# Optimization experiments

Hardware: AMD Instinct MI355X
Metric: run time of the kernel (lower is better)

## Reference

```python
import jax, jax.numpy as jnp
import numpy as np
import math

H = 0.1
SHIFTS = (1, 2, 4, 8)
INTERACTION_SCALE = 0.05
DEXP_ORDER = 4
EXP_TERMS = 8
BERNOULLI = (1.0, -0.5, 1.0 / 6.0, 0.0, -1.0 / 30.0)


def _gp_table():
    # Cl(3,0) geometric product structure constants, basis [1,e1,e2,e3,e12,e13,e23,e123]
    def sign(a, b):
        a >>= 1
        total = 0
        while a:
            total += bin(a & b).count('1')
            a >>= 1
        return -1.0 if total & 1 else 1.0
    masks = [0b000, 0b001, 0b010, 0b100, 0b011, 0b101, 0b110, 0b111]
    idx = {m: i for i, m in enumerate(masks)}
    M = np.zeros((8, 8, 8), np.float32)
    for i, a in enumerate(masks):
        for j, b in enumerate(masks):
            M[i, j, idx[a ^ b]] = sign(a, b)
    return M

GP_TABLE = jnp.asarray(_gp_table())


def gp(a, b):
    # Clifford geometric product over the trailing 8-dim multivector axis
    return jnp.einsum('...i,ijk,...j->...k', a, GP_TABLE, b)


def clifford_exp(u, terms=EXP_TERMS):
    ident = jnp.zeros_like(u).at[..., 0].set(1.0)
    res, term = ident, ident
    for n in range(1, terms):
        term = gp(term, u) / float(n)
        res = res + term
    return res


def dexp_inv(u, w, order=DEXP_ORDER):
    # dexp^{-1}_u(w) = sum_k B_k/k! * ad_u^k(w)
    res = BERNOULLI[0] * w
    adw = w
    for k in range(1, order + 1):
        adw = gp(u, adw) - gp(adw, u)
        c = BERNOULLI[k] / math.factorial(k)
        if c != 0.0:
            res = res + c * adw
    return res


def derivative_fn(y, t):
    # harmonic-oscillator phase-space field: dq = p, dp = -q
    d = jnp.zeros_like(y)
    d = d.at[..., 1:4].set(y[..., 4:7])
    d = d.at[..., 4:7].set(-y[..., 1:4])
    return d


def rolling_interaction(y):
    accum = jnp.zeros_like(y)
    for s in SHIFTS:
        accum = accum + gp(y, jnp.roll(y, -s, axis=-2)) / float(s)
    return INTERACTION_SCALE * accum / float(len(SHIFTS))


def vector_field(y, t):
    return derivative_fn(y, t) + rolling_interaction(y)


def left_multiply(u, y):
    return gp(clifford_exp(u), y)


def step(y, t, dt):
    zero = jnp.zeros_like(y)
    k1 = dexp_inv(zero, vector_field(left_multiply(zero, y), t))
    u2 = 0.5 * dt * k1
    k2 = dexp_inv(u2, vector_field(left_multiply(u2, y), t + 0.5 * dt))
    u3 = 0.5 * dt * k2
    k3 = dexp_inv(u3, vector_field(left_multiply(u3, y), t + 0.5 * dt))
    u4 = dt * k3
    k4 = dexp_inv(u4, vector_field(left_multiply(u4, y), t + dt))
    u = dt * (k1 + 2.0 * k2 + 2.0 * k3 + k4) / 6.0
    u = jnp.clip(jnp.nan_to_num(u, nan=0.0, posinf=1.0, neginf=-1.0), -1.0, 1.0)
    return left_multiply(u, y)


def setup_inputs() -> dict:
    key = jax.random.key(0)
    y = jax.random.normal(key, (32, 65536, 8), dtype=jnp.float32)
    t = jnp.zeros((), dtype=jnp.float32)
    return {"y": y, "t": t}


def reference(y, t):
    return step(y, t, jnp.asarray(H, dtype=y.dtype))
```

## Files before the change

kernel.cpp:

```cpp
#include <hip/hip_runtime.h>
#include <math.h>

#define CC   256
#define SP   8
#define NY   (CC + 33)
#define NZ   (CC + 25)
#define NK2  (CC + 17)
#define NK3  (CC + 9)
#define ISCL 0.0125f


__device__ __forceinline__ void cmul(float& orr, float& oi,
                                     float ar, float ai, float br, float bi) {
    orr = fmaf(ar, br, -(ai * bi));
    oi  = fmaf(ar, bi,   ai * br);
}
__device__ __forceinline__ void cmad(float& orr, float& oi,
                                     float ar, float ai, float br, float bi) {
    orr = fmaf(ar, br, fmaf(-ai, bi, orr));
    oi  = fmaf(ar, bi, fmaf( ai, br, oi));
}
__device__ __forceinline__ void cmsub(float& orr, float& oi,
                                      float ar, float ai, float br, float bi) {
    orr = fmaf(-ar, br, fmaf( ai, bi, orr));
    oi  = fmaf(-ar, bi, fmaf(-ai, br, oi));
}

__device__ __forceinline__ void mm2(const float* a, const float* b, float* o) {
    float r0,r1,r2,r3,r4,r5,r6,r7;
    cmul(r0,r1, a[0],a[1], b[0],b[1]); cmad(r0,r1, a[2],a[3], b[4],b[5]);
    cmul(r2,r3, a[0],a[1], b[2],b[3]); cmad(r2,r3, a[2],a[3], b[6],b[7]);
    cmul(r4,r5, a[4],a[5], b[0],b[1]); cmad(r4,r5, a[6],a[7], b[4],b[5]);
    cmul(r6,r7, a[4],a[5], b[2],b[3]); cmad(r6,r7, a[6],a[7], b[6],b[7]);
    o[0]=r0; o[1]=r1; o[2]=r2; o[3]=r3; o[4]=r4; o[5]=r5; o[6]=r6; o[7]=r7;
}

__device__ __forceinline__ void comm_core2(const float* u6,
        float w01r, float w01i, float w10r, float w10i,
        float dwr, float dwi, float* o6) {
    const float dar = 2.f * u6[0], dai = 2.f * u6[1];
    float ar, ai;
    cmul (ar, ai, u6[2],u6[3], w10r,w10i);
    cmsub(ar, ai, u6[4],u6[5], w01r,w01i);
    o6[0] = ar; o6[1] = ai;
    cmul (ar, ai, w01r,w01i, dar,dai);
    cmsub(ar, ai, u6[2],u6[3], dwr,dwi);
    o6[2] = ar; o6[3] = ai;
    cmul (ar, ai, u6[4],u6[5], dwr,dwi);
    cmsub(ar, ai, w10r,w10i, dar,dai);
    o6[4] = ar; o6[5] = ai;
}

__device__ __forceinline__ void dexpinv8(const float* k, const float* w,
                                         float s, float* o) {
    float u6[6];
    u6[0] = 0.5f*(k[0]-k[6]); u6[1] = 0.5f*(k[1]-k[7]);
    u6[2] = k[2]; u6[3] = k[3]; u6[4] = k[4]; u6[5] = k[5];
    float a1[6], a2[6];
    comm_core2(u6, w[2],w[3], w[4],w[5], w[0]-w[6], w[1]-w[7], a1);
    comm_core2(u6, a1[2],a1[3], a1[4],a1[5], 2.f*a1[0], 2.f*a1[1], a2);
    float wkr = fmaf(u6[0],u6[0], -(u6[1]*u6[1]));
    wkr = fmaf(u6[2], u6[4], wkr); wkr = fmaf(-u6[3], u6[5], wkr);
    float wki = 2.f*u6[0]*u6[1];
    wki = fmaf(u6[2], u6[5], wki); wki = fmaf(u6[3], u6[4], wki);
    const float s2  = s*s;
    const float c1  = -0.5f*s;
    const float c2  = s2*(1.f/12.f);
    const float c4m = -(s2*s2)*(1.f/180.f);
    const float gr = fmaf(c4m, wkr, c2), gi = c4m*wki;
    float acc[6];
#pragma unroll
    for (int p = 0; p < 3; ++p) {
        const float a2r = a2[2*p], a2i = a2[2*p+1];
        acc[2*p]   = fmaf(gr, a2r, fmaf(-gi, a2i, c1*a1[2*p]));
        acc[2*p+1] = fmaf(gr, a2i, fmaf( gi, a2r, c1*a1[2*p+1]));
    }
    o[0] = w[0] + acc[0]; o[1] = w[1] + acc[1];
    o[2] = w[2] + acc[2]; o[3] = w[3] + acc[3];
    o[4] = w[4] + acc[4]; o[5] = w[5] + acc[5];
    o[6] = w[6] - acc[0]; o[7] = w[7] - acc[1];
}

__device__ __forceinline__ void chstep(float& pr, float& pi,
                                       float wr, float wi, float K) {
    const float nr = fmaf(pr, wr, fmaf(-pi, wi, K));
    const float ni = fmaf(pr, wi, pi * wr);
    pr = nr; pi = ni;
}
template<bool FULL>
__device__ __forceinline__ void expm(const float* k, float s, float* o) {
    const float hs = 0.5f * s;
    const float c0r = hs*(k[0]+k[6]), c0i = hs*(k[1]+k[7]);
    const float v0r = hs*(k[0]-k[6]), v0i = hs*(k[1]-k[7]);
    const float v1r = s*k[2], v1i = s*k[3];
    const float v2r = s*k[4], v2i = s*k[5];
    float wr = fmaf(v0r, v0r, -(v0i*v0i));
    wr = fmaf(v1r, v2r, wr); wr = fmaf(-v1i, v2i, wr);
    float wi = 2.f*v0r*v0i;
    wi = fmaf(v1r, v2i, wi); wi = fmaf(v1i, v2r, wi);
    float Cr, Ci = 0.f, Sr, Si = 0.f;
    if (FULL) {
        Cr = 1.f/40320.f;
        chstep(Cr, Ci, wr, wi, 1.f/720.f);
        chstep(Cr, Ci, wr, wi, 1.f/24.f);
        chstep(Cr, Ci, wr, wi, 0.5f);
        chstep(Cr, Ci, wr, wi, 1.f);
        Sr = 1.f/362880.f;
        chstep(Sr, Si, wr, wi, 1.f/5040.f);
        chstep(Sr, Si, wr, wi, 1.f/120.f);
        chstep(Sr, Si, wr, wi, 1.f/6.f);
        chstep(Sr, Si, wr, wi, 1.f);
    } else {
        Cr = 1.f/24.f;
        chstep(Cr, Ci, wr, wi, 0.5f);
        chstep(Cr, Ci, wr, wi, 1.f);
        Sr = 1.f/120.f;
        chstep(Sr, Si, wr, wi, 1.f/6.f);
        chstep(Sr, Si, wr, wi, 1.f);
    }
    const float ex = __expf(c0r);
    const float cs = __cosf(c0i), sn = __sinf(c0i);
    const float er = ex*cs, ei = ex*sn;
    float p0r, p0i; cmul(p0r, p0i, Sr, Si, v0r, v0i);
    const float tr = Cr + p0r, ti = Ci + p0i;
    const float ur = Cr - p0r, ui = Ci - p0i;
    cmul(o[0], o[1], er, ei, tr, ti);
    cmul(o[6], o[7], er, ei, ur, ui);
    float qr, qi; cmul(qr, qi, er, ei, Sr, Si);
    cmul(o[2], o[3], qr, qi, v1r, v1i);
    cmul(o[4], o[5], qr, qi, v2r, v2i);
}

__device__ __forceinline__ int sbase(int e) { return (e << 3) ^ (e & 4); }

__device__ __forceinline__ void lds_load8(const float* buf, int e, float* o) {
    const int b = sbase(e);
    float4 a = *(const float4*)(buf + b);
    float4 c = *(const float4*)(buf + (b ^ 4));
    o[0] = a.x; o[1] = a.y; o[2] = a.z; o[3] = a.w;
    o[4] = c.x; o[5] = c.y; o[6] = c.z; o[7] = c.w;
}
__device__ __forceinline__ void lds_store8(float* buf, int e, const float* v) {
    const int b = sbase(e);
    *(float4*)(buf + b)       = make_float4(v[0], v[1], v[2], v[3]);
    *(float4*)(buf + (b ^ 4)) = make_float4(v[4], v[5], v[6], v[7]);
}

__device__ __forceinline__ void vf8_lds(const float* buf, int e, float* o) {
    float z0[8], t1[8], t2[8], t4[8], t8[8], bc[8], g[8];
    lds_load8(buf, e,     z0);
    lds_load8(buf, e + 1, t1);
    lds_load8(buf, e + 2, t2);
    lds_load8(buf, e + 4, t4);
    lds_load8(buf, e + 8, t8);
#pragma unroll
    for (int c = 0; c < 8; ++c)
        bc[c] = fmaf(0.125f, t8[c], fmaf(0.25f, t4[c], fmaf(0.5f, t2[c], t1[c])));
    mm2(z0, bc, g);
    const float Sr  = z0[2]+z0[4], Si  = z0[3]+z0[5];
    const float Ddr = z0[0]-z0[6], Ddi = z0[1]-z0[7];
    const float Tr  = z0[4]-z0[2], Ti  = z0[5]-z0[3];
    o[0] = fmaf(ISCL, g[0],  0.5f*Si);
    o[1] = fmaf(ISCL, g[1], -0.5f*Sr);
    o[2] = fmaf(ISCL, g[2],  0.5f*(Ddi+Ti));
    o[3] = fmaf(ISCL, g[3], -0.5f*(Ddr+Tr));
    o[4] = fmaf(ISCL, g[4],  0.5f*(Ddi-Ti));
    o[5] = fmaf(ISCL, g[5], -0.5f*(Ddr-Tr));
    o[6] = fmaf(ISCL, g[6], -0.5f*Si);
    o[7] = fmaf(ISCL, g[7],  0.5f*Sr);
}

__device__ __forceinline__ void zstage(const float* ybuf, float* zbuf, int e,
                                       const float* k, float scale) {
    float ex[8], yv[8], o[8];
    expm<false>(k, scale, ex);
    lds_load8(ybuf, e, yv);
    mm2(ex, yv, o);
    lds_store8(zbuf, e, o);
}

__device__ __forceinline__ void kstage(const float* zbuf, int e,
                                       const float* kin, float scale, float* kout) {
    float w[8];
    vf8_lds(zbuf, e, w);
    dexpinv8(kin, w, scale, kout);
}

__global__ __launch_bounds__(CC, 4)
void clifford_step_kernel(const float* __restrict__ y, float* __restrict__ out) {
    __shared__ __align__(16) float sy[NY * SP];
    __shared__ __align__(16) float sz[NZ * SP];

    const int tid   = threadIdx.x;
    const int row   = blockIdx.x >> 8;
    const int chunk = blockIdx.x & 255;
    const int base  = chunk * CC;
    const int bt    = (tid - ((blockIdx.x & 3) << 6)) & 255;
    const float* __restrict__ yrow = y + (size_t)row * 65536u * 8u;

    {
        const int g0 = (base + tid) & 65535;
        const float4* p = (const float4*)(yrow + (size_t)g0 * 8u);
        float4 A = p[0], B = p[1];
        const int s = sbase(tid);
        *(float4*)&sy[s]     = make_float4(A.x + A.w, B.w + B.x, A.y - B.y, B.z - A.z);
        *(float4*)&sy[s ^ 4] = make_float4(A.y + B.y, B.z + A.z, A.x - A.w, B.w - B.x);
        if (bt < NY - CC) {
            const int e  = CC + bt;
            const int g1 = (base + e) & 65535;
            const float4* q = (const float4*)(yrow + (size_t)g1 * 8u);
            float4 Cv = q[0], D = q[1];
            const int s2 = sbase(e);
            *(float4*)&sy[s2]     = make_float4(Cv.x + Cv.w, D.w + D.x, Cv.y - D.y, D.z - Cv.z);
            *(float4*)&sy[s2 ^ 4] = make_float4(Cv.y + D.y, D.z + Cv.z, Cv.x - Cv.w, D.w - D.x);
        }
    }
    __syncthreads();

    float ka[8], kb[8], uacc[8], kn[8];

    vf8_lds(sy, tid, ka);
#pragma unroll
    for (int c = 0; c < 8; ++c) uacc[c] = ka[c];
    if (bt < NZ - CC) vf8_lds(sy, CC + bt, kb);

    zstage(sy, sz, tid, ka, 0.05f);
    if (bt < NZ - CC) zstage(sy, sz, CC + bt, kb, 0.05f);
    __syncthreads();

    kstage(sz, tid, ka, 0.05f, kn);
#pragma unroll
    for (int c = 0; c < 8; ++c) { ka[c] = kn[c]; uacc[c] = fmaf(2.f, kn[c], uacc[c]); }
    if (bt < NK2 - CC) {
        kstage(sz, CC + bt, kb, 0.05f, kn);
#pragma unroll
        for (int c = 0; c < 8; ++c) kb[c] = kn[c];
    }
    __syncthreads();

    zstage(sy, sz, tid, ka, 0.05f);
    if (bt < NK2 - CC) zstage(sy, sz, CC + bt, kb, 0.05f);
    __syncthreads();

    kstage(sz, tid, ka, 0.05f, kn);
#pragma unroll
    for (int c = 0; c < 8; ++c) { ka[c] = kn[c]; uacc[c] = fmaf(2.f, kn[c], uacc[c]); }
    if (bt < NK3 - CC) {
        kstage(sz, CC + bt, kb, 0.05f, kn);
#pragma unroll
        for (int c = 0; c < 8; ++c) kb[c] = kn[c];
    }
    __syncthreads();

    zstage(sy, sz, tid, ka, 0.1f);
    if (bt < NK3 - CC) zstage(sy, sz, CC + bt, kb, 0.1f);
    __syncthreads();

    {
        const int e = tid;
        float w[8], k4[8], um[8], ex[8], yv[8], om[8];
        vf8_lds(sz, e, w);
        dexpinv8(ka, w, 0.1f, k4);

        const float s6 = 0.1f / 6.0f;
#pragma unroll
        for (int c = 0; c < 8; ++c)
            um[c] = s6 * (uacc[c] + k4[c]);
        float av[8];
        av[0] = 0.5f*(um[0]+um[6]); av[3] = 0.5f*(um[0]-um[6]);
        av[7] = 0.5f*(um[1]+um[7]); av[4] = 0.5f*(um[1]-um[7]);
        av[1] = 0.5f*(um[2]+um[4]); av[5] = 0.5f*(um[4]-um[2]);
        av[6] = 0.5f*(um[3]+um[5]); av[2] = 0.5f*(um[5]-um[3]);
#pragma unroll
        for (int c = 0; c < 8; ++c) {
            float v = av[c];
            if (isnan(v)) v = 0.f;
            av[c] = fmaxf(-1.f, fminf(v, 1.f));
        }
        um[0] = av[0]+av[3]; um[1] = av[7]+av[4];
        um[2] = av[1]-av[5]; um[3] = av[6]-av[2];
        um[4] = av[1]+av[5]; um[5] = av[6]+av[2];
        um[6] = av[0]-av[3]; um[7] = av[7]-av[4];

        expm<true>(um, 1.f, ex);
        lds_load8(sy, e, yv);
        mm2(ex, yv, om);

        float* dst = out + ((size_t)row * 65536u + (size_t)(base + e)) * 8u;
        ((float4*)dst)[0] = make_float4(0.5f*(om[0]+om[6]), 0.5f*(om[2]+om[4]),
                                        0.5f*(om[5]-om[3]), 0.5f*(om[0]-om[6]));
        ((float4*)dst)[1] = make_float4(0.5f*(om[1]-om[7]), 0.5f*(om[4]-om[2]),
                                        0.5f*(om[3]+om[5]), 0.5f*(om[1]+om[7]));
    }
}

extern "C" void kernel_launch(void* const* d_in, const int* in_sizes, int n_in,
                              void* d_out, int out_size, void* d_ws, size_t ws_size,
                              hipStream_t stream) {
    const float* y = (const float*)d_in[0];
    float* out = (float*)d_out;
    dim3 grid(32 * 256);
    dim3 block(CC);
    hipLaunchKernelGGL(clifford_step_kernel, grid, block, 0, stream, y, out);
}
```

Measured before the change: 83.50 us.

## Double-buffer stage LDS to drop barriers, approximate scalar exp, stream shift loads

```diff
diff --git a/kernel.cpp b/kernel.cpp
--- a/kernel.cpp
+++ b/kernel.cpp
@@ -99,6 +99,7 @@
     float wi = 2.f*v0r*v0i;
     wi = fmaf(v1r, v2i, wi); wi = fmaf(v1i, v2r, wi);
     float Cr, Ci = 0.f, Sr, Si = 0.f;
+    float er, ei;
     if (FULL) {
         Cr = 1.f/40320.f;
         chstep(Cr, Ci, wr, wi, 1.f/720.f);
@@ -110,6 +111,9 @@
         chstep(Sr, Si, wr, wi, 1.f/120.f);
         chstep(Sr, Si, wr, wi, 1.f/6.f);
         chstep(Sr, Si, wr, wi, 1.f);
+        const float ex = __expf(c0r);
+        er = ex * __cosf(c0i);
+        ei = ex * __sinf(c0i);
     } else {
         Cr = 1.f/24.f;
         chstep(Cr, Ci, wr, wi, 0.5f);
@@ -117,10 +121,13 @@
         Sr = 1.f/120.f;
         chstep(Sr, Si, wr, wi, 1.f/6.f);
         chstep(Sr, Si, wr, wi, 1.f);
-    }
-    const float ex = __expf(c0r);
-    const float cs = __cosf(c0i), sn = __sinf(c0i);
-    const float er = ex*cs, ei = ex*sn;
+        float t1r = fmaf(c0r, 1.f/3.f, 1.f), t1i = c0i * (1.f/3.f);
+        float t2r, t2i;
+        cmul(t2r, t2i, t1r, t1i, c0r, c0i);
+        t2r = fmaf(0.5f, t2r, 1.f); t2i *= 0.5f;
+        cmul(er, ei, t2r, t2i, c0r, c0i);
+        er += 1.f;
+    }
     float p0r, p0i; cmul(p0r, p0i, Sr, Si, v0r, v0i);
     const float tr = Cr + p0r, ti = Ci + p0i;
     const float ur = Cr - p0r, ui = Ci - p0i;
@@ -147,15 +154,18 @@
 }
 
 __device__ __forceinline__ void vf8_lds(const float* buf, int e, float* o) {
-    float z0[8], t1[8], t2[8], t4[8], t8[8], bc[8], g[8];
+    float z0[8], bc[8], t[8], g[8];
     lds_load8(buf, e,     z0);
-    lds_load8(buf, e + 1, t1);
-    lds_load8(buf, e + 2, t2);
-    lds_load8(buf, e + 4, t4);
-    lds_load8(buf, e + 8, t8);
-#pragma unroll
-    for (int c = 0; c < 8; ++c)
-        bc[c] = fmaf(0.125f, t8[c], fmaf(0.25f, t4[c], fmaf(0.5f, t2[c], t1[c])));
+    lds_load8(buf, e + 1, bc);
+    lds_load8(buf, e + 2, t);
+#pragma unroll
+    for (int c = 0; c < 8; ++c) bc[c] = fmaf(0.5f, t[c], bc[c]);
+    lds_load8(buf, e + 4, t);
+#pragma unroll
+    for (int c = 0; c < 8; ++c) bc[c] = fmaf(0.25f, t[c], bc[c]);
+    lds_load8(buf, e + 8, t);
+#pragma unroll
+    for (int c = 0; c < 8; ++c) bc[c] = fmaf(0.125f, t[c], bc[c]);
     mm2(z0, bc, g);
     const float Sr  = z0[2]+z0[4], Si  = z0[3]+z0[5];
     const float Ddr = z0[0]-z0[6], Ddi = z0[1]-z0[7];
@@ -188,8 +198,9 @@
 
 __global__ __launch_bounds__(CC, 4)
 void clifford_step_kernel(const float* __restrict__ y, float* __restrict__ out) {
-    __shared__ __align__(16) float sy[NY * SP];
-    __shared__ __align__(16) float sz[NZ * SP];
+    __shared__ __align__(16) float sy [NY  * SP];
+    __shared__ __align__(16) float szA[NZ  * SP];
+    __shared__ __align__(16) float szB[NK2 * SP];
 
     const int tid   = threadIdx.x;
     const int row   = blockIdx.x >> 8;
@@ -223,43 +234,38 @@
 #pragma unroll
     for (int c = 0; c < 8; ++c) uacc[c] = ka[c];
     if (bt < NZ - CC) vf8_lds(sy, CC + bt, kb);
-
-    zstage(sy, sz, tid, ka, 0.05f);
-    if (bt < NZ - CC) zstage(sy, sz, CC + bt, kb, 0.05f);
+    zstage(sy, szA, tid, ka, 0.05f);
+    if (bt < NZ - CC) zstage(sy, szA, CC + bt, kb, 0.05f);
     __syncthreads();
 
-    kstage(sz, tid, ka, 0.05f, kn);
+    kstage(szA, tid, ka, 0.05f, kn);
 #pragma unroll
     for (int c = 0; c < 8; ++c) { ka[c] = kn[c]; uacc[c] = fmaf(2.f, kn[c], uacc[c]); }
     if (bt < NK2 - CC) {
-        kstage(sz, CC + bt, kb, 0.05f, kn);
+        kstage(szA, CC + bt, kb, 0.05f, kn);
 #pragma unroll
         for (int c = 0; c < 8; ++c) kb[c] = kn[c];
     }
+    zstage(sy, szB, tid, ka, 0.05f);
+    if (bt < NK2 - CC) zstage(sy, szB, CC + bt, kb, 0.05f);
     __syncthreads();
 
-    zstage(sy, sz, tid, ka, 0.05f);
-    if (bt < NK2 - CC) zstage(sy, sz, CC + bt, kb, 0.05f);
-    __syncthreads();
-
-    kstage(sz, tid, ka, 0.05f, kn);
+    kstage(szB, tid, ka, 0.05f, kn);
 #pragma unroll
     for (int c = 0; c < 8; ++c) { ka[c] = kn[c]; uacc[c] = fmaf(2.f, kn[c], uacc[c]); }
     if (bt < NK3 - CC) {
-        kstage(sz, CC + bt, kb, 0.05f, kn);
+        kstage(szB, CC + bt, kb, 0.05f, kn);
 #pragma unroll
         for (int c = 0; c < 8; ++c) kb[c] = kn[c];
     }
-    __syncthreads();
-
-    zstage(sy, sz, tid, ka, 0.1f);
-    if (bt < NK3 - CC) zstage(sy, sz, CC + bt, kb, 0.1f);
+    zstage(sy, szA, tid, ka, 0.1f);
+    if (bt < NK3 - CC) zstage(sy, szA, CC + bt, kb, 0.1f);
     __syncthreads();
 
     {
         const int e = tid;
         float w[8], k4[8], um[8], ex[8], yv[8], om[8];
-        vf8_lds(sz, e, w);
+        vf8_lds(szA, e, w);
         dexpinv8(ka, w, 0.1f, k4);
 
         const float s6 = 0.1f / 6.0f;
```

Result: slower. 87.32 us (+4.6%).
